# Optimization experiments

Measured on AMD Instinct MI355X. Metric: run time of the kernel, lower is better.

## Reference

```python
import jax, jax.numpy as jnp
import numpy as np

OFFSET_FP32 = np.uint32(1064828928)  # L-mul exponent-bias correction constant for float32


def lmul_matmul(A, B):
    """Approximate A @ B (m,n)x(n,p) via integer-add-as-multiply on float bit patterns.

    Torch ref adds bit patterns in int64 then truncates with .to(torch.uint32),
    i.e. arithmetic mod 2**32 -- identical to plain uint32 wraparound addition,
    so we stay in uint32 and avoid needing x64 mode.
    """
    Au = jax.lax.bitcast_convert_type(A, jnp.uint32)          # (m, n)
    Bu = jax.lax.bitcast_convert_type(B, jnp.uint32)          # (n, p)
    prod_bits = Au[:, :, None] + Bu[None, :, :] - OFFSET_FP32  # (m, n, p), wraps mod 2^32
    prod = jax.lax.bitcast_convert_type(prod_bits, jnp.float32)
    return prod.sum(axis=1)                                    # (m, p)


def setup_inputs() -> dict:
    key = jax.random.key(0)
    k1, k2, k3 = jax.random.split(key, 3)
    m, n, p = 256, 512, 512
    x = jax.random.normal(k1, (m, n), dtype=jnp.float32)
    bound = 1.0 / np.sqrt(n)  # kaiming_uniform(a=sqrt(5)) -> U(-1/sqrt(fan_in), 1/sqrt(fan_in))
    weight = jax.random.uniform(k2, (p, n), dtype=jnp.float32, minval=-bound, maxval=bound)
    bias = jax.random.uniform(k3, (p,), dtype=jnp.float32, minval=-bound, maxval=bound)
    return {"x": x, "weight": weight, "bias": bias}


def reference(x, weight, bias):
    out = lmul_matmul(x, weight.T)
    return out + bias
```

## Files before the change

### kernel.cpp

```cpp
#include <hip/hip_runtime.h>
#include <stdint.h>


#define OFFSET_FP32 1064828928u

constexpr int M = 256;
constexpr int N = 512;
constexpr int P = 512;

constexpr int BP = 128;
constexpr int BM = 8;
constexpr int TM = 4;
constexpr int KS = 4;
constexpr int KT = N / KS;

__global__ __launch_bounds__(256) void lmul_linear_kernel(
    const uint32_t* __restrict__ xb,
    const uint32_t* __restrict__ wb,
    const float*    __restrict__ bias,
    float*          __restrict__ out)
{
    __shared__ uint32_t Bs[BP * KT];

    const int tid     = threadIdx.x;
    const int p_local = tid & (BP - 1);
    const int m_quad  = __builtin_amdgcn_readfirstlane(tid >> 7);

    const int p0 = blockIdx.y * BP;
    const int m0 = blockIdx.x * BM + m_quad * TM;
    const int k0 = blockIdx.z * KT;

    const int sg = tid & 31;
    const int sr = tid >> 5;
    const uint32_t* wbase = wb + (size_t)p0 * N + k0;
    #pragma unroll
    for (int j = 0; j < 16; ++j) {
        const int pp = sr + j * 8;
        uint4 v = *(const uint4*)(wbase + (size_t)pp * N + sg * 4);
        v.x -= OFFSET_FP32; v.y -= OFFSET_FP32;
        v.z -= OFFSET_FP32; v.w -= OFFSET_FP32;
        const int g = sg ^ (pp & 7);
        *(uint4*)&Bs[pp * KT + g * 4] = v;
    }
    __syncthreads();

    const uint32_t* xr0 = xb + (size_t)(m0 + 0) * N + k0;
    const uint32_t* xr1 = xb + (size_t)(m0 + 1) * N + k0;
    const uint32_t* xr2 = xb + (size_t)(m0 + 2) * N + k0;
    const uint32_t* xr3 = xb + (size_t)(m0 + 3) * N + k0;

    float acc[TM][4] = {};
    const uint32_t* brow = &Bs[p_local * KT];
    const int rot = p_local & 7;

    #pragma unroll 8
    for (int j = 0; j < KT / 4; ++j) {
        const uint4 b  = *(const uint4*)&brow[(j ^ rot) * 4];
        const uint4 a0 = *(const uint4*)(xr0 + j * 4);
        const uint4 a1 = *(const uint4*)(xr1 + j * 4);
        const uint4 a2 = *(const uint4*)(xr2 + j * 4);
        const uint4 a3 = *(const uint4*)(xr3 + j * 4);
        acc[0][0] += __uint_as_float(a0.x + b.x);
        acc[0][1] += __uint_as_float(a0.y + b.y);
        acc[0][2] += __uint_as_float(a0.z + b.z);
        acc[0][3] += __uint_as_float(a0.w + b.w);
        acc[1][0] += __uint_as_float(a1.x + b.x);
        acc[1][1] += __uint_as_float(a1.y + b.y);
        acc[1][2] += __uint_as_float(a1.z + b.z);
        acc[1][3] += __uint_as_float(a1.w + b.w);
        acc[2][0] += __uint_as_float(a2.x + b.x);
        acc[2][1] += __uint_as_float(a2.y + b.y);
        acc[2][2] += __uint_as_float(a2.z + b.z);
        acc[2][3] += __uint_as_float(a2.w + b.w);
        acc[3][0] += __uint_as_float(a3.x + b.x);
        acc[3][1] += __uint_as_float(a3.y + b.y);
        acc[3][2] += __uint_as_float(a3.z + b.z);
        acc[3][3] += __uint_as_float(a3.w + b.w);
    }

    const int p  = p0 + p_local;
    const float bv = (k0 == 0) ? bias[p] : 0.0f;
    #pragma unroll
    for (int r = 0; r < TM; ++r) {
        const float s = (acc[r][0] + acc[r][1]) + (acc[r][2] + acc[r][3]) + bv;
        atomicAdd(&out[(size_t)(m0 + r) * P + p], s);
    }
}

extern "C" void kernel_launch(void* const* d_in, const int* in_sizes, int n_in,
                              void* d_out, int out_size, void* d_ws, size_t ws_size,
                              hipStream_t stream) {
    const uint32_t* xb   = (const uint32_t*)d_in[0];
    const uint32_t* wb   = (const uint32_t*)d_in[1];
    const float*    bias = (const float*)d_in[2];
    float*          out  = (float*)d_out;

    hipMemsetAsync(d_out, 0, (size_t)out_size * sizeof(float), stream);

    dim3 grid(M / BM, P / BP, KS);
    dim3 block(256);
    lmul_linear_kernel<<<grid, block, 0, stream>>>(xb, wb, bias, out);
}
```

Measured before the change: 64.70 us.

## Replace atomic split-K accumulation with workspace partials and a reduce kernel

The split-K kernel now writes each K-slice's partial sums to its own plane in the workspace instead of atomically adding into the output. A second kernel sums the four planes with float4 loads and adds the bias, which also removes the output memset. This trades atomic traffic and the memset launch for an extra kernel launch plus writing and re-reading 4x M*P floats of workspace. Summation order becomes deterministic.

```diff
diff --git a/kernel.cpp b/kernel.cpp
--- a/kernel.cpp
+++ b/kernel.cpp
@@ -14,11 +14,10 @@
 constexpr int KS = 4;
 constexpr int KT = N / KS;
 
-__global__ __launch_bounds__(256) void lmul_linear_kernel(
+__global__ __launch_bounds__(256) void lmul_partial_kernel(
     const uint32_t* __restrict__ xb,
     const uint32_t* __restrict__ wb,
-    const float*    __restrict__ bias,
-    float*          __restrict__ out)
+    float*          __restrict__ pws)
 {
     __shared__ uint32_t Bs[BP * KT];
 
@@ -28,7 +27,8 @@
 
     const int p0 = blockIdx.y * BP;
     const int m0 = blockIdx.x * BM + m_quad * TM;
-    const int k0 = blockIdx.z * KT;
+    const int kz = blockIdx.z;
+    const int k0 = kz * KT;
 
     const int sg = tid & 31;
     const int sr = tid >> 5;
@@ -78,13 +78,36 @@
         acc[3][3] += __uint_as_float(a3.w + b.w);
     }
 
-    const int p  = p0 + p_local;
-    const float bv = (k0 == 0) ? bias[p] : 0.0f;
+    const int p = p0 + p_local;
+    float* plane = pws + (size_t)kz * M * P;
     #pragma unroll
     for (int r = 0; r < TM; ++r) {
-        const float s = (acc[r][0] + acc[r][1]) + (acc[r][2] + acc[r][3]) + bv;
-        atomicAdd(&out[(size_t)(m0 + r) * P + p], s);
+        plane[(size_t)(m0 + r) * P + p] =
+            (acc[r][0] + acc[r][1]) + (acc[r][2] + acc[r][3]);
     }
+}
+
+__global__ __launch_bounds__(256) void lmul_reduce_kernel(
+    const float* __restrict__ pws,
+    const float* __restrict__ bias,
+    float*       __restrict__ out)
+{
+    constexpr int MP4 = M * P / 4;
+    const int idx = blockIdx.x * 256 + threadIdx.x;
+
+    const float4* w4 = (const float4*)pws;
+    float4 s0 = w4[idx];
+    float4 s1 = w4[idx + MP4];
+    float4 s2 = w4[idx + 2 * MP4];
+    float4 s3 = w4[idx + 3 * MP4];
+    const float4 b4 = ((const float4*)bias)[idx & (P / 4 - 1)];
+
+    float4 r;
+    r.x = (s0.x + s1.x) + (s2.x + s3.x) + b4.x;
+    r.y = (s0.y + s1.y) + (s2.y + s3.y) + b4.y;
+    r.z = (s0.z + s1.z) + (s2.z + s3.z) + b4.z;
+    r.w = (s0.w + s1.w) + (s2.w + s3.w) + b4.w;
+    ((float4*)out)[idx] = r;
 }
 
 extern "C" void kernel_launch(void* const* d_in, const int* in_sizes, int n_in,
@@ -94,10 +117,11 @@
     const uint32_t* wb   = (const uint32_t*)d_in[1];
     const float*    bias = (const float*)d_in[2];
     float*          out  = (float*)d_out;
+    float*          pws  = (float*)d_ws;
 
-    hipMemsetAsync(d_out, 0, (size_t)out_size * sizeof(float), stream);
+    dim3 grid1(M / BM, P / BP, KS);
+    lmul_partial_kernel<<<grid1, dim3(256), 0, stream>>>(xb, wb, pws);
 
-    dim3 grid(M / BM, P / BP, KS);
-    dim3 block(256);
-    lmul_linear_kernel<<<grid, block, 0, stream>>>(xb, wb, bias, out);
+    dim3 grid2(M * P / 4 / 256);
+    lmul_reduce_kernel<<<grid2, dim3(256), 0, stream>>>(pws, bias, out);
 }
```

After: 65.64 us. No clear change (+1.4%).
